# Kernel tuning notes

Measured on AMD Instinct MI355X. Metric: run time of the kernel, lower is better.

The kernel has to match this reference:

```python
import jax, jax.numpy as jnp
import numpy as np

# Mamba2(d_model=256, headdim=32) defaults: d_state=128, d_conv=4, expand=2, ngroups=1, chunk=256
B, CIN, L = 8, 256, 1024
D_MODEL = CIN
D_INNER = 2 * D_MODEL            # expand=2 -> 512
HEADDIM = 32
NHEADS = D_INNER // HEADDIM      # 16
D_STATE = 128
D_CONV = 4
CONV_DIM = D_INNER + 2 * D_STATE             # 768 (ngroups=1)
D_IN_PROJ = 2 * D_INNER + 2 * D_STATE + NHEADS  # 1296
GN_GROUPS = 8
CHUNK = 256
EPS = 1e-5

def setup_inputs():
    key = jax.random.key(0)
    ks = jax.random.split(key, 8)
    x = jax.random.normal(ks[0], (B, CIN, L), jnp.float32)
    W_in = jax.random.normal(ks[1], (D_IN_PROJ, D_MODEL), jnp.float32) * 0.02
    conv_w = jax.random.normal(ks[2], (CONV_DIM, D_CONV), jnp.float32) * 0.2
    conv_b = jax.random.normal(ks[3], (CONV_DIM,), jnp.float32) * 0.02
    dt = jnp.exp(jax.random.uniform(ks[4], (NHEADS,)) * (jnp.log(0.1) - jnp.log(0.001)) + jnp.log(0.001))
    dt_bias = dt + jnp.log(-jnp.expm1(-dt))   # inverse softplus
    A_log = jnp.log(jax.random.uniform(ks[5], (NHEADS,), minval=1.0, maxval=16.0))
    Dp = jnp.ones((NHEADS,), jnp.float32)
    rms_w = jnp.ones((D_INNER,), jnp.float32)
    W_out = jax.random.normal(ks[6], (D_MODEL, D_INNER), jnp.float32) * 0.02
    gn_w = jnp.ones((CIN,), jnp.float32)
    gn_b = jnp.zeros((CIN,), jnp.float32)
    return dict(x=x, W_in=W_in, conv_w=conv_w, conv_b=conv_b, dt_bias=dt_bias,
                A_log=A_log, Dp=Dp, rms_w=rms_w, W_out=W_out, gn_w=gn_w, gn_b=gn_b)

def segsum(a):
    # a: (..., T) -> (..., T, T) with sum_{j<i<=t} a_i on/below diagonal, -inf above
    T = a.shape[-1]
    cs = jnp.cumsum(a, -1)
    d = cs[..., :, None] - cs[..., None, :]
    mask = jnp.tril(jnp.ones((T, T), bool))
    return jnp.where(mask, d, -jnp.inf)

def ssd(X, A, Bm, Cm):
    # X: (b,l,h,p) already dt-scaled; A: (b,l,h) = dt*A_cont; Bm,Cm: (b,l,n) (ngroups=1)
    b, l, h, p = X.shape
    n = Bm.shape[-1]
    c = l // CHUNK
    X = X.reshape(b, c, CHUNK, h, p)
    A = A.reshape(b, c, CHUNK, h).transpose(0, 3, 1, 2)      # (b,h,c,l)
    Bm = Bm.reshape(b, c, CHUNK, n)
    Cm = Cm.reshape(b, c, CHUNK, n)
    A_cs = jnp.cumsum(A, -1)                                  # (b,h,c,l)
    Lmat = jnp.exp(segsum(A))                                 # (b,h,c,l,l)
    Y_diag = jnp.einsum('bcln,bcsn,bhcls,bcshp->bclhp', Cm, Bm, Lmat, X)
    decay_states = jnp.exp(A_cs[..., -1:] - A_cs)             # (b,h,c,l)
    states = jnp.einsum('bcln,bhcl,bclhp->bchpn', Bm, decay_states, X)
    decay_chunk = jnp.exp(segsum(jnp.pad(A_cs[..., -1], ((0, 0), (0, 0), (1, 0)))))  # (b,h,c+1,c+1)
    states = jnp.concatenate([jnp.zeros_like(states[:, :1]), states], axis=1)        # (b,c+1,h,p,n)
    prev = jnp.einsum('bhzc,bchpn->bzhpn', decay_chunk, states)[:, :-1]              # (b,c,h,p,n)
    Y_off = jnp.einsum('bcln,bchpn,bhcl->bclhp', Cm, prev, jnp.exp(A_cs))
    return (Y_diag + Y_off).reshape(b, l, h, p)

def _forward(x, W_in, conv_w, conv_b, dt_bias, A_log, Dp, rms_w, W_out, gn_w, gn_b):
    u = jnp.transpose(x, (0, 2, 1))                           # (B,L,d_model)
    zxbcdt = u @ W_in.T                                       # (B,L,1296)
    z = zxbcdt[..., :D_INNER]
    xBC = zxbcdt[..., D_INNER:D_INNER + CONV_DIM]
    dt = jax.nn.softplus(zxbcdt[..., D_INNER + CONV_DIM:] + dt_bias)  # (B,L,H)
    # causal depthwise conv1d + SiLU
    xpad = jnp.pad(xBC, ((0, 0), (D_CONV - 1, 0), (0, 0)))
    xconv = conv_b + sum(conv_w[:, k] * xpad[:, k:k + L, :] for k in range(D_CONV))
    xconv = jax.nn.silu(xconv)
    xs = xconv[..., :D_INNER].reshape(B, L, NHEADS, HEADDIM)
    Bm = xconv[..., D_INNER:D_INNER + D_STATE]
    Cm = xconv[..., D_INNER + D_STATE:]
    A = -jnp.exp(A_log)                                       # (H,)
    Y = ssd(dt[..., None] * xs, dt * A, Bm, Cm)               # (B,L,H,P)
    Y = Y + xs * Dp[None, None, :, None]
    # gated RMSNorm (norm_before_gate=False): rmsnorm(y * silu(z)) * weight
    y = Y.reshape(B, L, D_INNER) * jax.nn.silu(z)
    y = y * jax.lax.rsqrt(jnp.mean(y * y, -1, keepdims=True) + EPS) * rms_w
    out = jnp.transpose(y @ W_out.T, (0, 2, 1))               # (B,C,L)
    # GroupNorm(8, C) over (channels_per_group, L)
    og = out.reshape(B, GN_GROUPS, CIN // GN_GROUPS, L)
    mu = og.mean((2, 3), keepdims=True)
    var = og.var((2, 3), keepdims=True)
    out = ((og - mu) * jax.lax.rsqrt(var + EPS)).reshape(B, CIN, L)
    out = out * gn_w[None, :, None] + gn_b[None, :, None]
    return out * jnp.tanh(jax.nn.softplus(out))               # Mish

def reference(x, W_in, conv_w, conv_b, dt_bias, A_log, Dp, rms_w, W_out, gn_w, gn_b):
    return _forward(x, W_in, conv_w, conv_b, dt_bias, A_log, Dp, rms_w, W_out, gn_w, gn_b)
```

## Files before the change

### kernel.cpp

```cpp
#include <hip/hip_runtime.h>
#include <hip/hip_bf16.h>
#include <math.h>

#define B_ 8
#define L_ 1024
#define DM 256
#define DI 512
#define HD 32
#define NH 16
#define DS 128
#define CDIM 768
#define NZX 1280
#define CH 256
#define NC 4
#define M_ (B_*L_)
#define EPSV 1e-5f

typedef short bf16x8 __attribute__((ext_vector_type(8)));
typedef float f32x4 __attribute__((ext_vector_type(4)));

#define OFF_ZX   0
#define SZ_ZX    (M_*NZX)
#define OFF_XC   (OFF_ZX+SZ_ZX)
#define SZ_XC    (M_*CDIM/2)
#define OFF_DT   (OFF_XC+SZ_XC)
#define SZ_DT    (M_*NH)
#define OFF_ACS  (OFF_DT+SZ_DT)
#define SZ_ACS   (B_*NC*NH*CH)
#define OFF_S0   (OFF_ACS+SZ_ACS)
#define SZ_S0    (B_*NC*CH*CH/2)
#define OFF_ST   (OFF_S0+SZ_S0)
#define SZ_ST    (B_*NC*NH*HD*DS)
#define OFF_PV   (OFF_ST+SZ_ST)
#define SZ_PV    SZ_ST
#define OFF_Y    (OFF_PV+SZ_PV)
#define SZ_Y     (M_*DI)
#define OFF_YNB  (OFF_Y+SZ_Y)
#define SZ_YNB   (M_*DI/2)
#define OFF_XBF  (OFF_YNB+SZ_YNB)
#define SZ_XBF   (M_*DM/2)
#define OFF_WBF  (OFF_XBF+SZ_XBF)
#define SZ_WBF   (1296*DM/2)
#define OFF_WOBF (OFF_WBF+SZ_WBF)
#define SZ_WOBF  (DM*DI/2)
#define OFF_GNP  (OFF_WOBF+SZ_WOBF)
#define SZ_GNP   (64*8*2)
#define OFF_GNS  (OFF_GNP+SZ_GNP)
#define SZ_GNS   (64*2)
#define OFF_BT   (OFF_GNS+SZ_GNS)
#define SZ_BT    (32*128*256/2)
#define OFF_XT   (OFF_BT+SZ_BT)
#define SZ_XT    (32*512*256/2)

__device__ __forceinline__ ushort f2bf(float v) {
  __hip_bfloat16 h = __float2bfloat16(v);
  return *(ushort*)&h;
}
__device__ __forceinline__ float bf2f(ushort u) {
  return __uint_as_float(((unsigned int)u) << 16);
}

__global__ void k_cast(const float* __restrict__ s, ushort* __restrict__ d, int n) {
  int i = blockIdx.x*256 + threadIdx.x;
  if (i < n) d[i] = f2bf(s[i]);
}

__global__ __launch_bounds__(256) void k_cast_x(const float* __restrict__ x,
                                                ushort* __restrict__ xbf) {
  __shared__ float Ts[64][65];
  const int k0 = blockIdx.x*64, l0 = blockIdx.y*64, b = blockIdx.z;
  const int t = threadIdx.x;
  for (int i = t; i < 4096; i += 256) {
    int kk = i>>6, ll = i&63;
    Ts[kk][ll] = x[(size_t)b*DM*L_ + (size_t)(k0+kk)*L_ + l0+ll];
  }
  __syncthreads();
  for (int i = t; i < 4096; i += 256) {
    int mm = i>>6, kk = i&63;
    xbf[(size_t)(b*L_ + l0+mm)*DM + k0+kk] = f2bf(Ts[kk][mm]);
  }
}

__global__ __launch_bounds__(256) void k_xpose(const ushort* __restrict__ xcb,
                                               ushort* __restrict__ dst,
                                               int src_col0, int ncols) {
  __shared__ ushort T[64][66];
  const int c0 = blockIdx.x*64, l0 = blockIdx.y*64, bc = blockIdx.z;
  const int t = threadIdx.x;
  const int base = bc*CH;
  for (int i = t; i < 4096; i += 256) {
    int lr = i>>6, cc = i&63;
    T[lr][cc] = xcb[(size_t)(base+l0+lr)*CDIM + src_col0 + c0+cc];
  }
  __syncthreads();
  for (int i = t; i < 4096; i += 256) {
    int cc = i>>6, lr = i&63;
    dst[((size_t)bc*ncols + c0+cc)*CH + l0+lr] = T[lr][cc];
  }
}

__global__ __launch_bounds__(256) void k_gemm_in_mfma(const ushort* __restrict__ xbf,
                                                      const ushort* __restrict__ wbf,
                                                      float* __restrict__ zx) {
  __shared__ ushort As[128*40];
  __shared__ ushort Bs[64*40];
  const int tid = threadIdx.x;
  const int n0 = blockIdx.x*64, m0 = blockIdx.y*128;
  const int wave = tid>>6, lane = tid&63;
  const int lr = lane&15, quad = lane>>4;
  const int KK = DM;
  f32x4 acc[2][4];
#pragma unroll
  for (int mi=0;mi<2;++mi)
#pragma unroll
    for (int ni=0;ni<4;++ni)
#pragma unroll
      for (int r=0;r<4;++r) acc[mi][ni][r] = 0.f;
  const int srow = tid>>2, sc = tid&3;
  for (int k0 = 0; k0 < KK; k0 += 32) {
    *(uint4*)&As[srow*40 + sc*8]      = *(const uint4*)(xbf + (size_t)(m0+srow)*KK    + k0 + sc*8);
    *(uint4*)&As[(srow+64)*40 + sc*8] = *(const uint4*)(xbf + (size_t)(m0+srow+64)*KK + k0 + sc*8);
    *(uint4*)&Bs[srow*40 + sc*8]      = *(const uint4*)(wbf + (size_t)(n0+srow)*KK    + k0 + sc*8);
    __syncthreads();
    bf16x8 af[2], bfr[4];
    const int ar = wave*32 + lr;
    af[0] = *(const bf16x8*)&As[ar*40 + quad*8];
    af[1] = *(const bf16x8*)&As[(ar+16)*40 + quad*8];
#pragma unroll
    for (int ni=0;ni<4;++ni) bfr[ni] = *(const bf16x8*)&Bs[(ni*16+lr)*40 + quad*8];
#pragma unroll
    for (int mi=0;mi<2;++mi)
#pragma unroll
      for (int ni=0;ni<4;++ni)
        acc[mi][ni] = __builtin_amdgcn_mfma_f32_16x16x32_bf16(af[mi], bfr[ni], acc[mi][ni], 0, 0, 0);
    __syncthreads();
  }
#pragma unroll
  for (int mi=0;mi<2;++mi) {
    int m = m0 + wave*32 + mi*16 + quad*4;
#pragma unroll
    for (int ni=0;ni<4;++ni) {
      int n = n0 + ni*16 + lr;
#pragma unroll
      for (int r=0;r<4;++r) zx[(size_t)(m+r)*NZX + n] = acc[mi][ni][r];
    }
  }
}

__global__ __launch_bounds__(256) void k_dt_direct(const float* __restrict__ x,
                                                   const float* __restrict__ W,
                                                   const float* __restrict__ dt_bias,
                                                   float* __restrict__ dtb) {
  __shared__ float Xs[256][16];
  __shared__ float Ws[16][257];
  const int t = threadIdx.x;
  const int bm = blockIdx.x*16;
  const int b = bm >> 10, l0 = bm & 1023;
  for (int i = t; i < 4096; i += 256) {
    int h = i>>8, k = i&255;
    Ws[h][k] = W[(size_t)(NZX+h)*DM + k];
  }
  for (int i = t; i < 4096; i += 256) {
    int k = i>>4, li = i&15;
    Xs[k][li] = x[(size_t)b*DM*L_ + (size_t)k*L_ + l0+li];
  }
  __syncthreads();
  const int h = t&15, li = t>>4;
  float acc = 0.f;
#pragma unroll 8
  for (int k = 0; k < 256; ++k) acc += Xs[k][li]*Ws[h][k];
  float v = acc + dt_bias[h];
  dtb[(size_t)bm*NH + t] = (v > 20.f) ? v : log1pf(expf(v));
}

__global__ __launch_bounds__(256) void k_conv(const float* __restrict__ zx,
                                              const float* __restrict__ cw,
                                              const float* __restrict__ cb,
                                              ushort* __restrict__ xcb) {
  const int j = blockIdx.x*256 + threadIdx.x;
  const int l0 = (blockIdx.y*4) & 1023;
  const int mb = (blockIdx.y*4) & ~1023;
  const float4 w = *(const float4*)&cw[j*4];
  const float bias = cb[j];
  float v[7];
#pragma unroll
  for (int i = 0; i < 7; ++i) {
    int ll = l0 - 3 + i;
    v[i] = (ll >= 0) ? zx[(size_t)(mb+ll)*NZX + DI + j] : 0.f;
  }
#pragma unroll
  for (int i = 0; i < 4; ++i) {
    float a = bias + w.x*v[i] + w.y*v[i+1] + w.z*v[i+2] + w.w*v[i+3];
    a = a / (1.f + expf(-a));
    xcb[(size_t)(mb+l0+i)*CDIM + j] = f2bf(a);
  }
}

__global__ __launch_bounds__(256) void k_s0_mfma(const ushort* __restrict__ xcb,
                                                 ushort* __restrict__ S0b) {
  const int lt = blockIdx.x, st = blockIdx.y, bc = blockIdx.z;
  if (st > lt) return;
  const int base = bc*CH;
  const int t = threadIdx.x;
  const int wave = t>>6, lane = t&63, lr = lane&15, quad = lane>>4;
  const int l = lt*64 + wave*16 + lr;
  f32x4 acc[4];
#pragma unroll
  for (int nt = 0; nt < 4; ++nt)
#pragma unroll
    for (int r = 0; r < 4; ++r) acc[nt][r] = 0.f;
#pragma unroll
  for (int ks = 0; ks < 4; ++ks) {
    bf16x8 af = *(const bf16x8*)(xcb + (size_t)(base+l)*CDIM + (DI+DS) + ks*32 + quad*8);
#pragma unroll
    for (int nt = 0; nt < 4; ++nt) {
      bf16x8 bf = *(const bf16x8*)(xcb + (size_t)(base + st*64 + nt*16 + lr)*CDIM + DI + ks*32 + quad*8);
      acc[nt] = __builtin_amdgcn_mfma_f32_16x16x32_bf16(af, bf, acc[nt], 0, 0, 0);
    }
  }
#pragma unroll
  for (int nt = 0; nt < 4; ++nt)
#pragma unroll
    for (int r = 0; r < 4; ++r)
      S0b[((size_t)bc*CH + lt*64 + wave*16 + quad*4 + r)*CH + st*64 + nt*16 + lr] = f2bf(acc[nt][r]);
}

__global__ __launch_bounds__(256) void k_states_mfma(const ushort* __restrict__ xtg,
                                                     const ushort* __restrict__ btg,
                                                     const float* __restrict__ dtb,
                                                     const float* __restrict__ A_log,
                                                     float* __restrict__ acs_g,
                                                     float* __restrict__ st) {
  __shared__ float acs[CH];
  __shared__ float wv[CH];
  __shared__ ushort Xw[32][264];
  const int t = threadIdx.x;
  const int bc = blockIdx.x, h = blockIdx.y;
  const int base = bc*CH;
  float dt_t = dtb[(size_t)(base+t)*NH + h];
  float An = -expf(A_log[h]);
  acs[t] = dt_t * An;
  __syncthreads();
  for (int off = 1; off < CH; off <<= 1) {
    float v = (t >= off) ? acs[t-off] : 0.f;
    __syncthreads();
    acs[t] += v;
    __syncthreads();
  }
  float alast = acs[CH-1];
  acs_g[((size_t)bc*NH + h)*CH + t] = acs[t];
  wv[t] = expf(alast - acs[t]) * dt_t;
  __syncthreads();
  {
    const int p = t>>3, lc = (t&7)*32;
    const ushort* xp = xtg + ((size_t)bc*DI + h*HD + p)*CH + lc;
#pragma unroll
    for (int c = 0; c < 4; ++c) {
      bf16x8 xv = *(const bf16x8*)(xp + c*8);
      bf16x8 o;
#pragma unroll
      for (int j = 0; j < 8; ++j)
        o[j] = (short)f2bf(bf2f((ushort)xv[j]) * wv[lc + c*8 + j]);
      *(bf16x8*)&Xw[p][lc + c*8] = o;
    }
  }
  __syncthreads();
  const int wave = t>>6, lane = t&63, lr = lane&15, quad = lane>>4;
  f32x4 acc[2][2];
#pragma unroll
  for (int mt=0;mt<2;++mt)
#pragma unroll
    for (int nt=0;nt<2;++nt)
#pragma unroll
      for (int r=0;r<4;++r) acc[mt][nt][r] = 0.f;
  const ushort* bp = btg + (size_t)bc*DS*CH;
#pragma unroll
  for (int k0 = 0; k0 < CH; k0 += 32) {
    bf16x8 a0 = *(const bf16x8*)&Xw[lr][k0 + quad*8];
    bf16x8 a1 = *(const bf16x8*)&Xw[16+lr][k0 + quad*8];
    bf16x8 b0 = *(const bf16x8*)(bp + (size_t)(wave*32 + lr)*CH + k0 + quad*8);
    bf16x8 b1 = *(const bf16x8*)(bp + (size_t)(wave*32 + 16 + lr)*CH + k0 + quad*8);
    acc[0][0] = __builtin_amdgcn_mfma_f32_16x16x32_bf16(a0, b0, acc[0][0], 0,0,0);
    acc[0][1] = __builtin_amdgcn_mfma_f32_16x16x32_bf16(a0, b1, acc[0][1], 0,0,0);
    acc[1][0] = __builtin_amdgcn_mfma_f32_16x16x32_bf16(a1, b0, acc[1][0], 0,0,0);
    acc[1][1] = __builtin_amdgcn_mfma_f32_16x16x32_bf16(a1, b1, acc[1][1], 0,0,0);
  }
  size_t sb = ((size_t)bc*NH + h)*HD*DS;
#pragma unroll
  for (int mt = 0; mt < 2; ++mt)
#pragma unroll
    for (int nt = 0; nt < 2; ++nt)
#pragma unroll
      for (int r = 0; r < 4; ++r)
        st[sb + (size_t)(mt*16 + quad*4 + r)*DS + wave*32 + nt*16 + lr] = acc[mt][nt][r];
}

__global__ void k_scan(const float* __restrict__ acs_g, const float* __restrict__ st,
                       float* __restrict__ pv) {
  const int b = blockIdx.x, h = blockIdx.y;
  const int t = threadIdx.x;
  float P[16];
#pragma unroll
  for (int i = 0; i < 16; ++i) P[i] = 0.f;
  for (int c = 0; c < NC; ++c) {
    size_t sb = ((size_t)(b*NC+c)*NH + h)*HD*DS;
    float T = acs_g[((size_t)(b*NC+c)*NH + h)*CH + (CH-1)];
    float ec = expf(T);
#pragma unroll
    for (int i = 0; i < 16; ++i) {
      size_t e = sb + (size_t)i*256 + t;
      pv[e] = P[i];
      P[i] = st[e] + ec * P[i];
    }
  }
}

__global__ __launch_bounds__(256) void k_y_mfma(const ushort* __restrict__ xcb,
    const float* __restrict__ dtb, const float* __restrict__ acs_g,
    const ushort* __restrict__ S0b, const float* __restrict__ pv,
    const float* __restrict__ Dp, float* __restrict__ Y) {
  __shared__ ushort Xt[32][280];
  __shared__ float acs[CH];
  __shared__ float dts[CH];
  __shared__ float E8[CH];
  const int t = threadIdx.x;
  const int bc = blockIdx.x, h = blockIdx.y;
  const int base = bc*CH;
  acs[t] = acs_g[((size_t)bc*NH + h)*CH + t];
  dts[t] = dtb[(size_t)(base+t)*NH + h];
  {
    const ushort* xp = xcb + (size_t)(base+t)*CDIM + h*HD;
    ushort tmp[32];
    *(uint4*)&tmp[0]  = *(const uint4*)(xp);
    *(uint4*)&tmp[8]  = *(const uint4*)(xp+8);
    *(uint4*)&tmp[16] = *(const uint4*)(xp+16);
    *(uint4*)&tmp[24] = *(const uint4*)(xp+24);
#pragma unroll
    for (int p = 0; p < 32; ++p) Xt[p][t] = tmp[p];
  }
  __syncthreads();
  E8[t] = expf(acs[t & ~7] - acs[t]) * dts[t];
  __syncthreads();
  const int wave = t>>6, lane = t&63, lr = lane&15, quad = lane>>4;
  f32x4 acc[4][2];
#pragma unroll
  for (int mt=0;mt<4;++mt)
#pragma unroll
    for (int nt=0;nt<2;++nt)
#pragma unroll
      for (int r=0;r<4;++r) acc[mt][nt][r] = 0.f;
  const size_t pb = ((size_t)bc*NH + h)*HD*DS;
#pragma unroll
  for (int ks = 0; ks < 4; ++ks) {
    bf16x8 bfr[2];
#pragma unroll
    for (int nt = 0; nt < 2; ++nt) {
      const float* pp = pv + pb + (size_t)(nt*16+lr)*DS + ks*32 + quad*8;
      float4 v0 = *(const float4*)pp;
      float4 v1 = *(const float4*)(pp+4);
      bf16x8 bb;
      bb[0]=(short)f2bf(v0.x); bb[1]=(short)f2bf(v0.y); bb[2]=(short)f2bf(v0.z); bb[3]=(short)f2bf(v0.w);
      bb[4]=(short)f2bf(v1.x); bb[5]=(short)f2bf(v1.y); bb[6]=(short)f2bf(v1.z); bb[7]=(short)f2bf(v1.w);
      bfr[nt] = bb;
    }
#pragma unroll
    for (int mt = 0; mt < 4; ++mt) {
      int l = wave*64 + mt*16 + lr;
      bf16x8 af = *(const bf16x8*)(xcb + (size_t)(base+l)*CDIM + (DI+DS) + ks*32 + quad*8);
      acc[mt][0] = __builtin_amdgcn_mfma_f32_16x16x32_bf16(af, bfr[0], acc[mt][0], 0,0,0);
      acc[mt][1] = __builtin_amdgcn_mfma_f32_16x16x32_bf16(af, bfr[1], acc[mt][1], 0,0,0);
    }
  }
#pragma unroll
  for (int mt = 0; mt < 4; ++mt)
#pragma unroll
    for (int r = 0; r < 4; ++r) {
      float e = expf(acs[wave*64 + mt*16 + quad*4 + r]);
      acc[mt][0][r] *= e;
      acc[mt][1][r] *= e;
    }
  float al[4];
#pragma unroll
  for (int mt = 0; mt < 4; ++mt) al[mt] = acs[wave*64 + mt*16 + lr];
  const int km3 = 2*wave + 1;
  for (int ks = 0; ks <= km3; ++ks) {
    const int sq = ks*32 + quad*8;
    const float as0 = acs[sq];
    const float4 e0 = *(const float4*)&E8[sq];
    const float4 e1 = *(const float4*)&E8[sq+4];
    const bf16x8 xb0 = *(const bf16x8*)&Xt[lr][sq];
    const bf16x8 xb1 = *(const bf16x8*)&Xt[16+lr][sq];
    const float ev[8] = {e0.x,e0.y,e0.z,e0.w,e1.x,e1.y,e1.z,e1.w};
#pragma unroll
    for (int mt = 0; mt < 4; ++mt) {
      if (ks > ((wave*64 + mt*16 + 15) >> 5)) continue;
      const int l = wave*64 + mt*16 + lr;
      const bf16x8 sb = *(const bf16x8*)(S0b + ((size_t)bc*CH + l)*CH + sq);
      const float el = expf(al[mt] - as0);
      bf16x8 mf;
#pragma unroll
      for (int j = 0; j < 8; ++j) {
        float v = (sq + j <= l) ? bf2f((ushort)sb[j]) * el * ev[j] : 0.f;
        mf[j] = (short)f2bf(v);
      }
      acc[mt][0] = __builtin_amdgcn_mfma_f32_16x16x32_bf16(mf, xb0, acc[mt][0], 0,0,0);
      acc[mt][1] = __builtin_amdgcn_mfma_f32_16x16x32_bf16(mf, xb1, acc[mt][1], 0,0,0);
    }
  }
  const float dph = Dp[h];
#pragma unroll
  for (int mt = 0; mt < 4; ++mt) {
    const int lb = wave*64 + mt*16 + quad*4;
#pragma unroll
    for (int nt = 0; nt < 2; ++nt) {
      const int p = nt*16 + lr;
#pragma unroll
      for (int r = 0; r < 4; ++r) {
        float xv = bf2f(Xt[p][lb+r]);
        Y[(size_t)(base+lb+r)*DI + h*HD + p] = acc[mt][nt][r] + dph*xv;
      }
    }
  }
}

__global__ __launch_bounds__(256) void k_rms(const float* __restrict__ zx,
                                             const float* __restrict__ Y,
                                             const float* __restrict__ rw,
                                             ushort* __restrict__ yn) {
  const int m = blockIdx.x, t = threadIdx.x;
  float z0 = zx[(size_t)m*NZX + t];
  float z1 = zx[(size_t)m*NZX + t + 256];
  float y0 = Y[(size_t)m*DI + t]       * z0 / (1.f + expf(-z0));
  float y1 = Y[(size_t)m*DI + t + 256] * z1 / (1.f + expf(-z1));
  float ss = y0*y0 + y1*y1;
#pragma unroll
  for (int off = 32; off > 0; off >>= 1) ss += __shfl_down(ss, off);
  __shared__ float red[4];
  __shared__ float sinv;
  if ((t & 63) == 0) red[t >> 6] = ss;
  __syncthreads();
  if (t == 0) sinv = rsqrtf((red[0]+red[1]+red[2]+red[3]) * (1.f/DI) + EPSV);
  __syncthreads();
  float inv = sinv;
  yn[(size_t)m*DI + t]       = f2bf(y0 * inv * rw[t]);
  yn[(size_t)m*DI + t + 256] = f2bf(y1 * inv * rw[t+256]);
}

__global__ __launch_bounds__(256) void k_gemm_out_mfma(const ushort* __restrict__ ynbf,
                                                       const ushort* __restrict__ wobf,
                                                       float* __restrict__ outp) {
  __shared__ ushort As[128*40];
  __shared__ ushort Bs[64*40];
  const int tid = threadIdx.x;
  const int n0 = blockIdx.x*64, m0 = blockIdx.y*128;
  const int wave = tid>>6, lane = tid&63;
  const int lr = lane&15, quad = lane>>4;
  const int KK = DI;
  f32x4 acc[2][4];
#pragma unroll
  for (int mi=0;mi<2;++mi)
#pragma unroll
    for (int ni=0;ni<4;++ni)
#pragma unroll
      for (int r=0;r<4;++r) acc[mi][ni][r] = 0.f;
  const int srow = tid>>2, sc = tid&3;
  for (int k0 = 0; k0 < KK; k0 += 32) {
    *(uint4*)&As[srow*40 + sc*8]      = *(const uint4*)(ynbf + (size_t)(m0+srow)*KK    + k0 + sc*8);
    *(uint4*)&As[(srow+64)*40 + sc*8] = *(const uint4*)(ynbf + (size_t)(m0+srow+64)*KK + k0 + sc*8);
    *(uint4*)&Bs[srow*40 + sc*8]      = *(const uint4*)(wobf + (size_t)(n0+srow)*KK    + k0 + sc*8);
    __syncthreads();
    bf16x8 af[2], bfr[4];
    const int ar = wave*32 + lr;
    af[0] = *(const bf16x8*)&As[ar*40 + quad*8];
    af[1] = *(const bf16x8*)&As[(ar+16)*40 + quad*8];
#pragma unroll
    for (int ni=0;ni<4;++ni) bfr[ni] = *(const bf16x8*)&Bs[(ni*16+lr)*40 + quad*8];
#pragma unroll
    for (int mi=0;mi<2;++mi)
#pragma unroll
      for (int ni=0;ni<4;++ni)
        acc[mi][ni] = __builtin_amdgcn_mfma_f32_16x16x32_bf16(af[mi], bfr[ni], acc[mi][ni], 0, 0, 0);
    __syncthreads();
  }
  const int b = m0 >> 10, l0 = m0 & 1023;
#pragma unroll
  for (int mi=0;mi<2;++mi) {
    int lb = l0 + wave*32 + mi*16 + quad*4;
#pragma unroll
    for (int ni=0;ni<4;++ni) {
      int n = n0 + ni*16 + lr;
      float4 v = make_float4(acc[mi][ni][0], acc[mi][ni][1], acc[mi][ni][2], acc[mi][ni][3]);
      *(float4*)&outp[(size_t)b*DM*L_ + (size_t)n*L_ + lb] = v;
    }
  }
}

__global__ __launch_bounds__(256) void k_gn_part(const float* __restrict__ o,
                                                 float2* __restrict__ part) {
  const int grp = blockIdx.x;
  const int sp  = blockIdx.y;
  const int t = threadIdx.x;
  size_t base = (size_t)grp*32*L_ + (size_t)sp*4096;
  float s = 0.f, ss = 0.f;
#pragma unroll
  for (int it = 0; it < 4; ++it) {
    float4 v = *(const float4*)&o[base + it*1024 + t*4];
    s  += v.x+v.y+v.z+v.w;
    ss += v.x*v.x+v.y*v.y+v.z*v.z+v.w*v.w;
  }
#pragma unroll
  for (int off = 32; off > 0; off >>= 1) { s += __shfl_down(s, off); ss += __shfl_down(ss, off); }
  __shared__ float rs[4], rss[4];
  if ((t & 63) == 0) { rs[t>>6] = s; rss[t>>6] = ss; }
  __syncthreads();
  if (t == 0) part[grp*8+sp] = make_float2(rs[0]+rs[1]+rs[2]+rs[3], rss[0]+rss[1]+rss[2]+rss[3]);
}

__global__ void k_gn_stats(const float2* __restrict__ part, float2* __restrict__ stats) {
  int g = threadIdx.x;
  float s = 0.f, ss = 0.f;
#pragma unroll
  for (int i = 0; i < 8; ++i) { float2 p = part[g*8+i]; s += p.x; ss += p.y; }
  float mean = s * (1.f/(32.f*L_));
  float var  = ss * (1.f/(32.f*L_)) - mean*mean;
  stats[g] = make_float2(mean, rsqrtf(var + EPSV));
}

__global__ __launch_bounds__(256) void k_gn_apply(const float2* __restrict__ stats,
                                                  const float* __restrict__ gw,
                                                  const float* __restrict__ gb,
                                                  float* __restrict__ o) {
  const int ch = blockIdx.x & 255, b = blockIdx.x >> 8;
  const int t = threadIdx.x;
  float2 st = stats[b*8 + (ch>>5)];
  const float mean = st.x, inv = st.y;
  const float w = gw[ch], bb = gb[ch];
  size_t base = (size_t)blockIdx.x * L_;
  float4 v = *(const float4*)&o[base + t*4];
  float r[4] = {v.x, v.y, v.z, v.w};
#pragma unroll
  for (int j = 0; j < 4; ++j) {
    float u = (r[j] - mean) * inv * w + bb;
    float m;
    if (u > 15.f) m = u;
    else {
      float e = expf(u);
      float a = 1.f + e;
      float a2 = a*a;
      m = u * (a2 - 1.f) / (a2 + 1.f);
    }
    r[j] = m;
  }
  *(float4*)&o[base + t*4] = make_float4(r[0], r[1], r[2], r[3]);
}

extern "C" void kernel_launch(void* const* d_in, const int* in_sizes, int n_in,
                              void* d_out, int out_size, void* d_ws, size_t ws_size,
                              hipStream_t stream) {
  const float* x       = (const float*)d_in[0];
  const float* W_in    = (const float*)d_in[1];
  const float* conv_w  = (const float*)d_in[2];
  const float* conv_b  = (const float*)d_in[3];
  const float* dt_bias = (const float*)d_in[4];
  const float* A_log   = (const float*)d_in[5];
  const float* Dp      = (const float*)d_in[6];
  const float* rms_w   = (const float*)d_in[7];
  const float* W_out   = (const float*)d_in[8];
  const float* gn_w    = (const float*)d_in[9];
  const float* gn_b    = (const float*)d_in[10];
  float* out = (float*)d_out;
  float* ws  = (float*)d_ws;

  float*  zx    = ws + OFF_ZX;
  ushort* xcb   = (ushort*)(ws + OFF_XC);
  float*  dtb   = ws + OFF_DT;
  float*  acs   = ws + OFF_ACS;
  ushort* S0b   = (ushort*)(ws + OFF_S0);
  float*  st    = ws + OFF_ST;
  float*  pv    = ws + OFF_PV;
  float*  Ybuf  = ws + OFF_Y;
  ushort* ynbf  = (ushort*)(ws + OFF_YNB);
  ushort* xbf   = (ushort*)(ws + OFF_XBF);
  ushort* wbf   = (ushort*)(ws + OFF_WBF);
  ushort* wobf  = (ushort*)(ws + OFF_WOBF);
  float2* gnp   = (float2*)(ws + OFF_GNP);
  float2* gns   = (float2*)(ws + OFF_GNS);
  ushort* btg   = (ushort*)(ws + OFF_BT);
  ushort* xtg   = (ushort*)(ws + OFF_XT);

  k_cast_x       <<<dim3(4, 16, 8), 256, 0, stream>>>(x, xbf);
  k_cast         <<<dim3((1296*DM+255)/256), 256, 0, stream>>>(W_in, wbf, 1296*DM);
  k_cast         <<<dim3((DM*DI+255)/256), 256, 0, stream>>>(W_out, wobf, DM*DI);
  k_gemm_in_mfma <<<dim3(NZX/64, M_/128), 256, 0, stream>>>(xbf, wbf, zx);
  k_dt_direct    <<<dim3(M_/16), 256, 0, stream>>>(x, W_in, dt_bias, dtb);
  k_conv         <<<dim3(3, M_/4), 256, 0, stream>>>(zx, conv_w, conv_b, xcb);
  k_xpose        <<<dim3(2, 4, B_*NC), 256, 0, stream>>>(xcb, btg, DI, DS);
  k_xpose        <<<dim3(8, 4, B_*NC), 256, 0, stream>>>(xcb, xtg, 0, DI);
  k_s0_mfma      <<<dim3(4, 4, B_*NC), 256, 0, stream>>>(xcb, S0b);
  k_states_mfma  <<<dim3(B_*NC, NH), 256, 0, stream>>>(xtg, btg, dtb, A_log, acs, st);
  k_scan         <<<dim3(B_, NH), 256, 0, stream>>>(acs, st, pv);
  k_y_mfma       <<<dim3(B_*NC, NH), 256, 0, stream>>>(xcb, dtb, acs, S0b, pv, Dp, Ybuf);
  k_rms          <<<dim3(M_), 256, 0, stream>>>(zx, Ybuf, rms_w, ynbf);
  k_gemm_out_mfma<<<dim3(DM/64, M_/128), 256, 0, stream>>>(ynbf, wobf, out);
  k_gn_part      <<<dim3(64, 8), 256, 0, stream>>>(out, gnp);
  k_gn_stats     <<<dim3(1), 64, 0, stream>>>(gnp, gns);
  k_gn_apply     <<<dim3(B_*DM), 256, 0, stream>>>(gns, gn_w, gn_b, out);
}
```

Baseline: 205.6 us.

## Store intermediates in bf16, fuse GroupNorm stats into out GEMM, drop x transpose

The zx projection output and the SSD Y output are now stored as bf16 instead of fp32, which halves their write and read traffic in the conv and RMS-norm kernels. GroupNorm partial sums are computed in the output GEMM epilogue and accumulated with atomics. This removes the separate partial-sum and stats kernels and their re-read of the output. The states kernel reads x directly from the conv buffer with per-thread row loads, so the second transpose kernel is gone. In exchange there is extra bf16 rounding on z and Y, atomic ordering nondeterminism, and an added zeroing launch.

```diff
diff --git a/kernel.cpp b/kernel.cpp
--- a/kernel.cpp
+++ b/kernel.cpp
@@ -20,7 +20,7 @@
 typedef float f32x4 __attribute__((ext_vector_type(4)));
 
 #define OFF_ZX   0
-#define SZ_ZX    (M_*NZX)
+#define SZ_ZX    (M_*NZX/2)
 #define OFF_XC   (OFF_ZX+SZ_ZX)
 #define SZ_XC    (M_*CDIM/2)
 #define OFF_DT   (OFF_XC+SZ_XC)
@@ -34,7 +34,7 @@
 #define OFF_PV   (OFF_ST+SZ_ST)
 #define SZ_PV    SZ_ST
 #define OFF_Y    (OFF_PV+SZ_PV)
-#define SZ_Y     (M_*DI)
+#define SZ_Y     (M_*DI/2)
 #define OFF_YNB  (OFF_Y+SZ_Y)
 #define SZ_YNB   (M_*DI/2)
 #define OFF_XBF  (OFF_YNB+SZ_YNB)
@@ -44,13 +44,9 @@
 #define OFF_WOBF (OFF_WBF+SZ_WBF)
 #define SZ_WOBF  (DM*DI/2)
 #define OFF_GNP  (OFF_WOBF+SZ_WOBF)
-#define SZ_GNP   (64*8*2)
-#define OFF_GNS  (OFF_GNP+SZ_GNP)
-#define SZ_GNS   (64*2)
-#define OFF_BT   (OFF_GNS+SZ_GNS)
+#define SZ_GNP   (64*2)
+#define OFF_BT   (OFF_GNP+SZ_GNP)
 #define SZ_BT    (32*128*256/2)
-#define OFF_XT   (OFF_BT+SZ_BT)
-#define SZ_XT    (32*512*256/2)
 
 __device__ __forceinline__ ushort f2bf(float v) {
   __hip_bfloat16 h = __float2bfloat16(v);
@@ -58,6 +54,10 @@
 }
 __device__ __forceinline__ float bf2f(ushort u) {
   return __uint_as_float(((unsigned int)u) << 16);
+}
+
+__global__ void k_zero_gnp(float2* __restrict__ gnp) {
+  gnp[threadIdx.x] = make_float2(0.f, 0.f);
 }
 
 __global__ void k_cast(const float* __restrict__ s, ushort* __restrict__ d, int n) {
@@ -101,7 +101,7 @@
 
 __global__ __launch_bounds__(256) void k_gemm_in_mfma(const ushort* __restrict__ xbf,
                                                       const ushort* __restrict__ wbf,
-                                                      float* __restrict__ zx) {
+                                                      ushort* __restrict__ zxb) {
   __shared__ ushort As[128*40];
   __shared__ ushort Bs[64*40];
   const int tid = threadIdx.x;
@@ -142,7 +142,7 @@
     for (int ni=0;ni<4;++ni) {
       int n = n0 + ni*16 + lr;
 #pragma unroll
-      for (int r=0;r<4;++r) zx[(size_t)(m+r)*NZX + n] = acc[mi][ni][r];
+      for (int r=0;r<4;++r) zxb[(size_t)(m+r)*NZX + n] = f2bf(acc[mi][ni][r]);
     }
   }
 }
@@ -173,7 +173,7 @@
   dtb[(size_t)bm*NH + t] = (v > 20.f) ? v : log1pf(expf(v));
 }
 
-__global__ __launch_bounds__(256) void k_conv(const float* __restrict__ zx,
+__global__ __launch_bounds__(256) void k_conv(const ushort* __restrict__ zxb,
                                               const float* __restrict__ cw,
                                               const float* __restrict__ cb,
                                               ushort* __restrict__ xcb) {
@@ -186,7 +186,7 @@
 #pragma unroll
   for (int i = 0; i < 7; ++i) {
     int ll = l0 - 3 + i;
-    v[i] = (ll >= 0) ? zx[(size_t)(mb+ll)*NZX + DI + j] : 0.f;
+    v[i] = (ll >= 0) ? bf2f(zxb[(size_t)(mb+ll)*NZX + DI + j]) : 0.f;
   }
 #pragma unroll
   for (int i = 0; i < 4; ++i) {
@@ -225,14 +225,13 @@
       S0b[((size_t)bc*CH + lt*64 + wave*16 + quad*4 + r)*CH + st*64 + nt*16 + lr] = f2bf(acc[nt][r]);
 }
 
-__global__ __launch_bounds__(256) void k_states_mfma(const ushort* __restrict__ xtg,
+__global__ __launch_bounds__(256) void k_states_mfma(const ushort* __restrict__ xcb,
                                                      const ushort* __restrict__ btg,
                                                      const float* __restrict__ dtb,
                                                      const float* __restrict__ A_log,
                                                      float* __restrict__ acs_g,
                                                      float* __restrict__ st) {
   __shared__ float acs[CH];
-  __shared__ float wv[CH];
   __shared__ ushort Xw[32][264];
   const int t = threadIdx.x;
   const int bc = blockIdx.x, h = blockIdx.y;
@@ -249,20 +248,16 @@
   }
   float alast = acs[CH-1];
   acs_g[((size_t)bc*NH + h)*CH + t] = acs[t];
-  wv[t] = expf(alast - acs[t]) * dt_t;
-  __syncthreads();
+  float w = expf(alast - acs[t]) * dt_t;
   {
-    const int p = t>>3, lc = (t&7)*32;
-    const ushort* xp = xtg + ((size_t)bc*DI + h*HD + p)*CH + lc;
-#pragma unroll
-    for (int c = 0; c < 4; ++c) {
-      bf16x8 xv = *(const bf16x8*)(xp + c*8);
-      bf16x8 o;
-#pragma unroll
-      for (int j = 0; j < 8; ++j)
-        o[j] = (short)f2bf(bf2f((ushort)xv[j]) * wv[lc + c*8 + j]);
-      *(bf16x8*)&Xw[p][lc + c*8] = o;
-    }
+    const ushort* xp = xcb + (size_t)(base+t)*CDIM + h*HD;
+    ushort tmp[32];
+    *(uint4*)&tmp[0]  = *(const uint4*)(xp);
+    *(uint4*)&tmp[8]  = *(const uint4*)(xp+8);
+    *(uint4*)&tmp[16] = *(const uint4*)(xp+16);
+    *(uint4*)&tmp[24] = *(const uint4*)(xp+24);
+#pragma unroll
+    for (int p = 0; p < 32; ++p) Xw[p][t] = f2bf(bf2f(tmp[p]) * w);
   }
   __syncthreads();
   const int wave = t>>6, lane = t&63, lr = lane&15, quad = lane>>4;
@@ -318,7 +313,7 @@
 __global__ __launch_bounds__(256) void k_y_mfma(const ushort* __restrict__ xcb,
     const float* __restrict__ dtb, const float* __restrict__ acs_g,
     const ushort* __restrict__ S0b, const float* __restrict__ pv,
-    const float* __restrict__ Dp, float* __restrict__ Y) {
+    const float* __restrict__ Dp, ushort* __restrict__ Yb) {
   __shared__ ushort Xt[32][280];
   __shared__ float acs[CH];
   __shared__ float dts[CH];
@@ -417,21 +412,21 @@
 #pragma unroll
       for (int r = 0; r < 4; ++r) {
         float xv = bf2f(Xt[p][lb+r]);
-        Y[(size_t)(base+lb+r)*DI + h*HD + p] = acc[mt][nt][r] + dph*xv;
+        Yb[(size_t)(base+lb+r)*DI + h*HD + p] = f2bf(acc[mt][nt][r] + dph*xv);
       }
     }
   }
 }
 
-__global__ __launch_bounds__(256) void k_rms(const float* __restrict__ zx,
-                                             const float* __restrict__ Y,
+__global__ __launch_bounds__(256) void k_rms(const ushort* __restrict__ zxb,
+                                             const ushort* __restrict__ Yb,
                                              const float* __restrict__ rw,
                                              ushort* __restrict__ yn) {
   const int m = blockIdx.x, t = threadIdx.x;
-  float z0 = zx[(size_t)m*NZX + t];
-  float z1 = zx[(size_t)m*NZX + t + 256];
-  float y0 = Y[(size_t)m*DI + t]       * z0 / (1.f + expf(-z0));
-  float y1 = Y[(size_t)m*DI + t + 256] * z1 / (1.f + expf(-z1));
+  float z0 = bf2f(zxb[(size_t)m*NZX + t]);
+  float z1 = bf2f(zxb[(size_t)m*NZX + t + 256]);
+  float y0 = bf2f(Yb[(size_t)m*DI + t])       * z0 / (1.f + expf(-z0));
+  float y1 = bf2f(Yb[(size_t)m*DI + t + 256]) * z1 / (1.f + expf(-z1));
   float ss = y0*y0 + y1*y1;
 #pragma unroll
   for (int off = 32; off > 0; off >>= 1) ss += __shfl_down(ss, off);
@@ -448,7 +443,8 @@
 
 __global__ __launch_bounds__(256) void k_gemm_out_mfma(const ushort* __restrict__ ynbf,
                                                        const ushort* __restrict__ wobf,
-                                                       float* __restrict__ outp) {
+                                                       float* __restrict__ outp,
+                                                       float2* __restrict__ gnp) {
   __shared__ ushort As[128*40];
   __shared__ ushort Bs[64*40];
   const int tid = threadIdx.x;
@@ -483,6 +479,7 @@
     __syncthreads();
   }
   const int b = m0 >> 10, l0 = m0 & 1023;
+  float s0=0.f, ss0=0.f, s1=0.f, ss1=0.f;
 #pragma unroll
   for (int mi=0;mi<2;++mi) {
     int lb = l0 + wave*32 + mi*16 + quad*4;
@@ -491,49 +488,39 @@
       int n = n0 + ni*16 + lr;
       float4 v = make_float4(acc[mi][ni][0], acc[mi][ni][1], acc[mi][ni][2], acc[mi][ni][3]);
       *(float4*)&outp[(size_t)b*DM*L_ + (size_t)n*L_ + lb] = v;
-    }
-  }
-}
-
-__global__ __launch_bounds__(256) void k_gn_part(const float* __restrict__ o,
-                                                 float2* __restrict__ part) {
-  const int grp = blockIdx.x;
-  const int sp  = blockIdx.y;
-  const int t = threadIdx.x;
-  size_t base = (size_t)grp*32*L_ + (size_t)sp*4096;
-  float s = 0.f, ss = 0.f;
-#pragma unroll
-  for (int it = 0; it < 4; ++it) {
-    float4 v = *(const float4*)&o[base + it*1024 + t*4];
-    s  += v.x+v.y+v.z+v.w;
-    ss += v.x*v.x+v.y*v.y+v.z*v.z+v.w*v.w;
-  }
-#pragma unroll
-  for (int off = 32; off > 0; off >>= 1) { s += __shfl_down(s, off); ss += __shfl_down(ss, off); }
-  __shared__ float rs[4], rss[4];
-  if ((t & 63) == 0) { rs[t>>6] = s; rss[t>>6] = ss; }
-  __syncthreads();
-  if (t == 0) part[grp*8+sp] = make_float2(rs[0]+rs[1]+rs[2]+rs[3], rss[0]+rss[1]+rss[2]+rss[3]);
-}
-
-__global__ void k_gn_stats(const float2* __restrict__ part, float2* __restrict__ stats) {
-  int g = threadIdx.x;
-  float s = 0.f, ss = 0.f;
-#pragma unroll
-  for (int i = 0; i < 8; ++i) { float2 p = part[g*8+i]; s += p.x; ss += p.y; }
-  float mean = s * (1.f/(32.f*L_));
-  float var  = ss * (1.f/(32.f*L_)) - mean*mean;
-  stats[g] = make_float2(mean, rsqrtf(var + EPSV));
-}
-
-__global__ __launch_bounds__(256) void k_gn_apply(const float2* __restrict__ stats,
+      float ps = v.x+v.y+v.z+v.w;
+      float pq = v.x*v.x+v.y*v.y+v.z*v.z+v.w*v.w;
+      if (ni < 2) { s0 += ps; ss0 += pq; } else { s1 += ps; ss1 += pq; }
+    }
+  }
+#pragma unroll
+  for (int off = 32; off > 0; off >>= 1) {
+    s0 += __shfl_down(s0, off); ss0 += __shfl_down(ss0, off);
+    s1 += __shfl_down(s1, off); ss1 += __shfl_down(ss1, off);
+  }
+  __shared__ float red[4][4];
+  if (lane == 0) { red[wave][0]=s0; red[wave][1]=ss0; red[wave][2]=s1; red[wave][3]=ss1; }
+  __syncthreads();
+  if (tid == 0) {
+    float S0=0,Q0=0,S1=0,Q1=0;
+#pragma unroll
+    for (int wv2 = 0; wv2 < 4; ++wv2) { S0+=red[wv2][0]; Q0+=red[wv2][1]; S1+=red[wv2][2]; Q1+=red[wv2][3]; }
+    int g0 = b*8 + (n0>>5);
+    atomicAdd(&gnp[g0].x, S0);   atomicAdd(&gnp[g0].y, Q0);
+    atomicAdd(&gnp[g0+1].x, S1); atomicAdd(&gnp[g0+1].y, Q1);
+  }
+}
+
+__global__ __launch_bounds__(256) void k_gn_apply(const float2* __restrict__ gnp,
                                                   const float* __restrict__ gw,
                                                   const float* __restrict__ gb,
                                                   float* __restrict__ o) {
   const int ch = blockIdx.x & 255, b = blockIdx.x >> 8;
   const int t = threadIdx.x;
-  float2 st = stats[b*8 + (ch>>5)];
-  const float mean = st.x, inv = st.y;
+  float2 p = gnp[b*8 + (ch>>5)];
+  const float mean = p.x * (1.f/(32.f*L_));
+  const float var  = p.y * (1.f/(32.f*L_)) - mean*mean;
+  const float inv  = rsqrtf(var + EPSV);
   const float w = gw[ch], bb = gb[ch];
   size_t base = (size_t)blockIdx.x * L_;
   float4 v = *(const float4*)&o[base + t*4];
@@ -571,38 +558,34 @@
   float* out = (float*)d_out;
   float* ws  = (float*)d_ws;
 
-  float*  zx    = ws + OFF_ZX;
+  ushort* zxb   = (ushort*)(ws + OFF_ZX);
   ushort* xcb   = (ushort*)(ws + OFF_XC);
   float*  dtb   = ws + OFF_DT;
   float*  acs   = ws + OFF_ACS;
   ushort* S0b   = (ushort*)(ws + OFF_S0);
   float*  st    = ws + OFF_ST;
   float*  pv    = ws + OFF_PV;
-  float*  Ybuf  = ws + OFF_Y;
+  ushort* Ybb   = (ushort*)(ws + OFF_Y);
   ushort* ynbf  = (ushort*)(ws + OFF_YNB);
   ushort* xbf   = (ushort*)(ws + OFF_XBF);
   ushort* wbf   = (ushort*)(ws + OFF_WBF);
   ushort* wobf  = (ushort*)(ws + OFF_WOBF);
   float2* gnp   = (float2*)(ws + OFF_GNP);
-  float2* gns   = (float2*)(ws + OFF_GNS);
   ushort* btg   = (ushort*)(ws + OFF_BT);
-  ushort* xtg   = (ushort*)(ws + OFF_XT);
-
+
+  k_zero_gnp     <<<dim3(1), 64, 0, stream>>>(gnp);
   k_cast_x       <<<dim3(4, 16, 8), 256, 0, stream>>>(x, xbf);
   k_cast         <<<dim3((1296*DM+255)/256), 256, 0, stream>>>(W_in, wbf, 1296*DM);
   k_cast         <<<dim3((DM*DI+255)/256), 256, 0, stream>>>(W_out, wobf, DM*DI);
-  k_gemm_in_mfma <<<dim3(NZX/64, M_/128), 256, 0, stream>>>(xbf, wbf, zx);
+  k_gemm_in_mfma <<<dim3(NZX/64, M_/128), 256, 0, stream>>>(xbf, wbf, zxb);
   k_dt_direct    <<<dim3(M_/16), 256, 0, stream>>>(x, W_in, dt_bias, dtb);
-  k_conv         <<<dim3(3, M_/4), 256, 0, stream>>>(zx, conv_w, conv_b, xcb);
+  k_conv         <<<dim3(3, M_/4), 256, 0, stream>>>(zxb, conv_w, conv_b, xcb);
   k_xpose        <<<dim3(2, 4, B_*NC), 256, 0, stream>>>(xcb, btg, DI, DS);
-  k_xpose        <<<dim3(8, 4, B_*NC), 256, 0, stream>>>(xcb, xtg, 0, DI);
   k_s0_mfma      <<<dim3(4, 4, B_*NC), 256, 0, stream>>>(xcb, S0b);
-  k_states_mfma  <<<dim3(B_*NC, NH), 256, 0, stream>>>(xtg, btg, dtb, A_log, acs, st);
+  k_states_mfma  <<<dim3(B_*NC, NH), 256, 0, stream>>>(xcb, btg, dtb, A_log, acs, st);
   k_scan         <<<dim3(B_, NH), 256, 0, stream>>>(acs, st, pv);
-  k_y_mfma       <<<dim3(B_*NC, NH), 256, 0, stream>>>(xcb, dtb, acs, S0b, pv, Dp, Ybuf);
-  k_rms          <<<dim3(M_), 256, 0, stream>>>(zx, Ybuf, rms_w, ynbf);
-  k_gemm_out_mfma<<<dim3(DM/64, M_/128), 256, 0, stream>>>(ynbf, wobf, out);
-  k_gn_part      <<<dim3(64, 8), 256, 0, stream>>>(out, gnp);
-  k_gn_stats     <<<dim3(1), 64, 0, stream>>>(gnp, gns);
-  k_gn_apply     <<<dim3(B_*DM), 256, 0, stream>>>(gns, gn_w, gn_b, out);
-}
+  k_y_mfma       <<<dim3(B_*NC, NH), 256, 0, stream>>>(xcb, dtb, acs, S0b, pv, Dp, Ybb);
+  k_rms          <<<dim3(M_), 256, 0, stream>>>(zxb, Ybb, rms_w, ynbf);
+  k_gemm_out_mfma<<<dim3(DM/64, M_/128), 256, 0, stream>>>(ynbf, wobf, out, gnp);
+  k_gn_apply     <<<dim3(B_*DM), 256, 0, stream>>>(gnp, gn_w, gn_b, out);
+}
```

Measured after the change: 197.4 us. 4.0% less time.
